# Kernel tuning notes

Hardware: AMD Instinct MI355X
Metric: run time of the kernel (lower is better)

The kernel has to match this reference:

```python
import jax, jax.numpy as jnp
import numpy as np
import math

C = 1.0
IN_FEATURES = 512
SCALE = 1.0 / math.sqrt(IN_FEATURES)  # 1/sqrt(input_size) * lr_mul, lr_mul=1
LR_MUL = 1.0
GAIN = math.sqrt(2.0)
EPS = 1e-5       # clamp epsilon used by hyptorch-style pmath
PROJ_EPS = 1e-3  # boundary epsilon for project()


def _norm(x):
    return jnp.linalg.norm(x, axis=-1, keepdims=True)


def _artanh(x):
    return jnp.arctanh(jnp.clip(x, -1.0 + EPS, 1.0 - EPS))


def _project(x, c):
    sqrt_c = c ** 0.5
    norm = jnp.maximum(_norm(x), EPS)
    maxnorm = (1.0 - PROJ_EPS) / sqrt_c
    return jnp.where(norm > maxnorm, x / norm * maxnorm, x)


def _expmap0(u, c):
    sqrt_c = c ** 0.5
    u_norm = jnp.maximum(_norm(u), EPS)
    return jnp.tanh(sqrt_c * u_norm) * u / (sqrt_c * u_norm)


def _mobius_add(x, y, c):
    x2 = jnp.sum(x * x, axis=-1, keepdims=True)
    y2 = jnp.sum(y * y, axis=-1, keepdims=True)
    xy = jnp.sum(x * y, axis=-1, keepdims=True)
    num = (1.0 + 2.0 * c * xy + c * y2) * x + (1.0 - c * x2) * y
    denom = 1.0 + 2.0 * c * xy + c * c * x2 * y2
    return num / (denom + EPS)


def _mobius_matvec(m, x, c):
    # m: [out, in], x: [N, in]
    sqrt_c = c ** 0.5
    x_norm = jnp.maximum(_norm(x), EPS)
    mx = x @ m.T  # [N, out]
    mx_norm = jnp.maximum(_norm(mx), EPS)
    res = jnp.tanh(mx_norm / x_norm * _artanh(sqrt_c * x_norm)) * mx / (mx_norm * sqrt_c)
    zero_row = jnp.all(mx == 0, axis=-1, keepdims=True)
    return jnp.where(zero_row, jnp.zeros_like(res), res)


def _mobius_scalar_mult(x, r, c):
    sqrt_c = c ** 0.5
    x_norm = jnp.maximum(_norm(x), EPS)
    return jnp.tanh(r * _artanh(sqrt_c * x_norm)) * x / (x_norm * sqrt_c)


def setup_inputs() -> dict:
    key = jax.random.key(0)
    k1, k2, k3 = jax.random.split(key, 3)
    N, D_IN, D_OUT = 131072, 512, 512
    # scale x so points lie well inside the unit Poincare ball (norm ~ 0.45)
    x = jax.random.normal(k1, (N, D_IN), dtype=jnp.float32) * 0.02
    weight = jax.random.normal(k2, (D_OUT, D_IN), dtype=jnp.float32)
    bias = jax.random.normal(k3, (D_OUT,), dtype=jnp.float32) * 0.01
    return {"x": x, "weight": weight, "bias": bias}


def reference(x, weight, bias):
    c = C
    mv = _mobius_matvec(weight * SCALE, x, c)
    b = _expmap0(bias * LR_MUL, c)
    out = _project(_mobius_add(mv, b[None, :], c), c)
    out = jax.nn.leaky_relu(out, 0.2)
    out = _mobius_scalar_mult(out, GAIN, c)
    return out
```

## Files before the change

kernel.cpp:

```cpp
#include <hip/hip_runtime.h>
#include <math.h>

#define EPSV 1e-5f
#define SCALE_W 0.0441941738241592f
#define GAIN_R 1.4142135623730951f

typedef __attribute__((ext_vector_type(8))) short bf16x8;
typedef __attribute__((ext_vector_type(4))) float f32x4;
typedef __attribute__((ext_vector_type(4))) unsigned int u32x4;

static __device__ __forceinline__ unsigned short f2bf(float f) {
  union { float f; unsigned int u; } v; v.f = f;
  unsigned int r = v.u + 0x7FFFu + ((v.u >> 16) & 1u);
  return (unsigned short)(r >> 16);
}

#define GLD_LDS16(gsrc, ldst)                                                                      \
  __builtin_amdgcn_global_load_lds((const __attribute__((address_space(1))) unsigned int*)(gsrc),  \
                                   (__attribute__((address_space(3))) unsigned int*)(ldst), 16, 0, 0)

#define LBAR() do {                                          \
  asm volatile("s_waitcnt lgkmcnt(0)" ::: "memory");         \
  __builtin_amdgcn_sched_barrier(0);                         \
  __builtin_amdgcn_s_barrier();                              \
  __builtin_amdgcn_sched_barrier(0);                         \
} while (0)

#define VMCNT(N) do {                                        \
  asm volatile("s_waitcnt vmcnt(" #N ")" ::: "memory");      \
  __builtin_amdgcn_sched_barrier(0);                         \
} while (0)

__global__ void bias_expmap_k(const float* __restrict__ bias, float* __restrict__ bexp,
                              float* __restrict__ y2out) {
  __shared__ float part[8];
  int t = threadIdx.x;
  float bv = bias[t];
  float s = bv * bv;
  s += __shfl_xor(s, 1);  s += __shfl_xor(s, 2);  s += __shfl_xor(s, 4);
  s += __shfl_xor(s, 8);  s += __shfl_xor(s, 16); s += __shfl_xor(s, 32);
  if ((t & 63) == 0) part[t >> 6] = s;
  __syncthreads();
  float tot = 0.f;
#pragma unroll
  for (int i = 0; i < 8; ++i) tot += part[i];
  float un = fmaxf(sqrtf(tot), EPSV);
  float th = tanhf(un);
  bexp[t] = th * bv / un;
  if (t == 0) *y2out = th * th;
}

__global__ void pack_weight_k(const float* __restrict__ w, unsigned short* __restrict__ wsB) {
  int e = blockIdx.x * 256 + threadIdx.x;
  int o = e >> 9;
  int k = e & 511;
  int ks = k >> 5, kk = k & 31;
  int lgr = kk >> 3, j = kk & 7;
  int colhi = o >> 4, l15 = o & 15;
  int dst = ((ks * 32 + colhi) * 64 + lgr * 16 + l15) * 8 + j;
  wsB[dst] = f2bf(w[e] * SCALE_W);
}

#define RB 80
#define ABUF 5120
#define BOFF 10240
#define BBUF 32768
#define SCR 75776
#define SMEMSZ 80896

__global__ __launch_bounds__(256, 2)
void hyp_main_k(const float* __restrict__ x, const unsigned short* __restrict__ wsB,
                const float* __restrict__ bexp, const float* __restrict__ y2p,
                float* __restrict__ out, int tilesPerBlk) {
  extern __shared__ char smem[];
  const int tid  = threadIdx.x;
  const int lane = tid & 63;
  const int wave = tid >> 6;
  const int l15  = lane & 15;
  const int lgr  = lane >> 4;
  const int srow = tid >> 2;
  const int sq   = tid & 3;

  float* xn2      = (float*)(smem + SCR);
  float* pS2      = (float*)(smem + SCR + 256);
  float* pSB      = (float*)(smem + SCR + 1280);
  float* g12      = (float*)(smem + SCR + 2304);
  float* bexp_lds = (float*)(smem + SCR + 2816);
  float* y2l      = (float*)(smem + SCR + 4864);

  f32x4 acc[4][8];
#pragma unroll
  for (int mf = 0; mf < 4; ++mf)
#pragma unroll
    for (int nf = 0; nf < 8; ++nf) acc[mf][nf] = f32x4{0.f, 0.f, 0.f, 0.f};

  const long base = (long)blockIdx.x * tilesPerBlk;
  const int U = tilesPerBlk * 16;
  float xss = 0.f;
  f32x4 stA, stB;

  {
    float2 bc = *(const float2*)(bexp + tid * 2);
    *(float2*)(bexp_lds + tid * 2) = bc;
    if (tid == 0) *y2l = *y2p;
    const float* p = x + (size_t)(base * 64 + srow) * 512 + sq * 8;
    f32x4 a = *(const f32x4*)p;
    f32x4 b = *(const f32x4*)(p + 4);
    xss += a[0]*a[0] + a[1]*a[1] + a[2]*a[2] + a[3]*a[3];
    xss += b[0]*b[0] + b[1]*b[1] + b[2]*b[2] + b[3]*b[3];
    u32x4 pk;
    pk[0] = (unsigned int)f2bf(a[0]) | ((unsigned int)f2bf(a[1]) << 16);
    pk[1] = (unsigned int)f2bf(a[2]) | ((unsigned int)f2bf(a[3]) << 16);
    pk[2] = (unsigned int)f2bf(b[0]) | ((unsigned int)f2bf(b[1]) << 16);
    pk[3] = (unsigned int)f2bf(b[2]) | ((unsigned int)f2bf(b[3]) << 16);
    *(u32x4*)(smem + srow * RB + sq * 16) = pk;
#pragma unroll
    for (int i = 0; i < 8; ++i)
      GLD_LDS16((const char*)wsB + (wave * 8 + i) * 1024 + lane * 16,
                smem + BOFF + (wave * 8 + i) * 1024);
  }
  LBAR();

#pragma unroll 1
  for (int t = 0; t < U; ++t) {
    const int cur = t & 1, nxt = cur ^ 1;

    {
      const int gu = (t + 1 < U) ? t + 1 : U - 1;
      const float* p = x + (size_t)((base + (gu >> 4)) * 64 + srow) * 512 + (gu & 15) * 32 + sq * 8;
      stA = *(const f32x4*)p;
      stB = *(const f32x4*)(p + 4);
    }
    {
      const char* bs = (const char*)wsB + (size_t)((t + 1) & 15) * 32768;
      char* bd = smem + BOFF + nxt * BBUF;
#pragma unroll
      for (int i = 0; i < 8; ++i)
        GLD_LDS16(bs + (wave * 8 + i) * 1024 + lane * 16, bd + (wave * 8 + i) * 1024);
    }
    if (t > 0 && (t & 15) == 0) { VMCNT(42); } else { VMCNT(10); }

    {
      const char* ab = smem + cur * ABUF + l15 * RB + lgr * 16;
      const char* bb = smem + BOFF + cur * BBUF + (wave * 8) * 1024 + lane * 16;
      bf16x8 xf[4], wf[8];
#pragma unroll
      for (int mf = 0; mf < 4; ++mf) xf[mf] = *(const bf16x8*)(ab + mf * (16 * RB));
#pragma unroll
      for (int nf = 0; nf < 8; ++nf) wf[nf] = *(const bf16x8*)(bb + nf * 1024);
      __builtin_amdgcn_s_setprio(1);
#pragma unroll
      for (int mf = 0; mf < 4; ++mf)
#pragma unroll
        for (int nf = 0; nf < 8; ++nf)
          acc[mf][nf] = __builtin_amdgcn_mfma_f32_16x16x32_bf16(wf[nf], xf[mf], acc[mf][nf], 0, 0, 0);
      __builtin_amdgcn_s_setprio(0);
    }

    if ((t & 15) == 15) {
      const long trow = (base + (t >> 4)) * 64;

      float xs = xss;
      xs += __shfl_xor(xs, 1); xs += __shfl_xor(xs, 2);
      if (sq == 0) xn2[srow] = xs;
      xss = 0.f;

      f32x4 bvv[8];
#pragma unroll
      for (int nf = 0; nf < 8; ++nf)
        bvv[nf] = *(const f32x4*)(bexp_lds + wave * 128 + nf * 16 + lgr * 4);
      const float y2 = *y2l;

      float s2[4], sb[4];
#pragma unroll
      for (int mf = 0; mf < 4; ++mf) {
        s2[mf] = 0.f; sb[mf] = 0.f;
#pragma unroll
        for (int nf = 0; nf < 8; ++nf)
#pragma unroll
          for (int j = 0; j < 4; ++j) {
            float v = acc[mf][nf][j];
            s2[mf] += v * v;
            sb[mf] += v * bvv[nf][j];
          }
        s2[mf] += __shfl_xor(s2[mf], 16); s2[mf] += __shfl_xor(s2[mf], 32);
        sb[mf] += __shfl_xor(sb[mf], 16); sb[mf] += __shfl_xor(sb[mf], 32);
      }
      if (lane < 16) {
#pragma unroll
        for (int mf = 0; mf < 4; ++mf) {
          pS2[(mf * 16 + l15) * 4 + wave] = s2[mf];
          pSB[(mf * 16 + l15) * 4 + wave] = sb[mf];
        }
      }
      LBAR();

      if (tid < 64) {
        int r = tid;
        float S2 = 0.f, SB = 0.f;
#pragma unroll
        for (int i = 0; i < 4; ++i) { S2 += pS2[r * 4 + i]; SB += pSB[r * 4 + i]; }
        float y2s = *y2l;
        float xn  = fmaxf(sqrtf(xn2[r]), EPSV);
        float mxn = fmaxf(sqrtf(S2), EPSV);
        float f = tanhf((mxn / xn) * atanhf(fminf(xn, 1.f - EPSV))) / mxn;
        float xy = f * SB;
        float x2 = f * f * S2;
        float den = 1.f + 2.f * xy + x2 * y2s + EPSV;
        float g1 = (1.f + 2.f * xy + y2s) * f / den;
        float g2 = (1.f - x2) / den;
        float n1sq = g1 * g1 * S2 + 2.f * g1 * g2 * SB + g2 * g2 * y2s;
        float n1 = fmaxf(sqrtf(fmaxf(n1sq, 0.f)), EPSV);
        if (n1 > 0.999f) { float sc = 0.999f / n1; g1 *= sc; g2 *= sc; }
        g12[r * 2] = g1; g12[r * 2 + 1] = g2;
      }
      LBAR();

      float n2p[4];
#pragma unroll
      for (int mf = 0; mf < 4; ++mf) {
        float g1 = g12[(mf * 16 + l15) * 2], g2 = g12[(mf * 16 + l15) * 2 + 1];
        n2p[mf] = 0.f;
#pragma unroll
        for (int nf = 0; nf < 8; ++nf)
#pragma unroll
          for (int j = 0; j < 4; ++j) {
            float v = g1 * acc[mf][nf][j] + g2 * bvv[nf][j];
            v = v > 0.f ? v : 0.2f * v;
            acc[mf][nf][j] = v;
            n2p[mf] += v * v;
          }
        n2p[mf] += __shfl_xor(n2p[mf], 16); n2p[mf] += __shfl_xor(n2p[mf], 32);
      }
      if (lane < 16) {
#pragma unroll
        for (int mf = 0; mf < 4; ++mf) pS2[(mf * 16 + l15) * 4 + wave] = n2p[mf];
      }
      LBAR();

      if (tid < 64) {
        int r = tid;
        float sn = 0.f;
#pragma unroll
        for (int i = 0; i < 4; ++i) sn += pS2[r * 4 + i];
        float n2 = fmaxf(sqrtf(sn), EPSV);
        xn2[r] = tanhf(GAIN_R * atanhf(fminf(n2, 1.f - EPSV))) / n2;
      }
      LBAR();

#pragma unroll
      for (int mf = 0; mf < 4; ++mf) {
        float tm = xn2[mf * 16 + l15];
#pragma unroll
        for (int nf = 0; nf < 8; ++nf) {
          f32x4 o = acc[mf][nf];
          o[0] *= tm; o[1] *= tm; o[2] *= tm; o[3] *= tm;
          *(f32x4*)(out + (size_t)(trow + mf * 16 + l15) * 512 +
                    wave * 128 + nf * 16 + lgr * 4) = o;
          acc[mf][nf] = f32x4{0.f, 0.f, 0.f, 0.f};
        }
      }
    }

    if ((t & 15) == 15) { VMCNT(40); } else { VMCNT(8); }

    {
      f32x4 a = stA, b = stB;
      xss += a[0]*a[0] + a[1]*a[1] + a[2]*a[2] + a[3]*a[3];
      xss += b[0]*b[0] + b[1]*b[1] + b[2]*b[2] + b[3]*b[3];
      u32x4 pk;
      pk[0] = (unsigned int)f2bf(a[0]) | ((unsigned int)f2bf(a[1]) << 16);
      pk[1] = (unsigned int)f2bf(a[2]) | ((unsigned int)f2bf(a[3]) << 16);
      pk[2] = (unsigned int)f2bf(b[0]) | ((unsigned int)f2bf(b[1]) << 16);
      pk[3] = (unsigned int)f2bf(b[2]) | ((unsigned int)f2bf(b[3]) << 16);
      *(u32x4*)(smem + nxt * ABUF + srow * RB + sq * 16) = pk;
    }
    LBAR();
  }
}

extern "C" void kernel_launch(void* const* d_in, const int* in_sizes, int n_in,
                              void* d_out, int out_size, void* d_ws, size_t ws_size,
                              hipStream_t stream) {
  const float* x    = (const float*)d_in[0];
  const float* w    = (const float*)d_in[1];
  const float* bias = (const float*)d_in[2];
  float* out = (float*)d_out;

  unsigned short* wsB = (unsigned short*)d_ws;
  float* bexp = (float*)((char*)d_ws + 524288);
  float* y2p  = (float*)((char*)d_ws + 524288 + 2048);

  bias_expmap_k<<<dim3(1), dim3(512), 0, stream>>>(bias, bexp, y2p);
  pack_weight_k<<<dim3(1024), dim3(256), 0, stream>>>(w, wsB);

  const int nrows  = in_sizes[0] / 512;
  const int ntiles = nrows / 64;
  const int nblk   = 512;
  const int tpb    = ntiles / nblk;
  hyp_main_k<<<dim3(nblk), dim3(256), SMEMSZ, stream>>>(x, wsB, bexp, y2p, out, tpb);
}
```

Baseline: 177.2 us.

## Deepen x prefetch to a 4-stage register ring and use hardware bf16 pack

The main loop now keeps a four-deep register ring of prefetched x fragments instead of a single stage, so global loads of x are issued several k-steps ahead. The loop is split into an outer per-tile loop with a fully unrolled 16-step inner loop, which makes the ring and buffer indices compile-time constants. The barrier moves to the start of each step with a fixed vmcnt wait. The bf16 conversion switches from a software round-to-nearest routine to the v_cvt_pk_bf16_f32 instruction. The deeper ring holds more live registers, which may lower occupancy, and the full unroll enlarges code size.

Result: slower. 441.0 us (+148.9%).

```diff
diff --git a/kernel.cpp b/kernel.cpp
--- a/kernel.cpp
+++ b/kernel.cpp
@@ -13,6 +13,12 @@
   union { float f; unsigned int u; } v; v.f = f;
   unsigned int r = v.u + 0x7FFFu + ((v.u >> 16) & 1u);
   return (unsigned short)(r >> 16);
+}
+
+static __device__ __forceinline__ unsigned int cvtpk(float lo, float hi) {
+  unsigned int r;
+  asm("v_cvt_pk_bf16_f32 %0, %1, %2" : "=v"(r) : "v"(lo), "v"(hi));
+  return r;
 }
 
 #define GLD_LDS16(gsrc, ldst)                                                                      \
@@ -30,6 +36,8 @@
   asm volatile("s_waitcnt vmcnt(" #N ")" ::: "memory");      \
   __builtin_amdgcn_sched_barrier(0);                         \
 } while (0)
+
+#define SBAR() __builtin_amdgcn_sched_barrier(0)
 
 __global__ void bias_expmap_k(const float* __restrict__ bias, float* __restrict__ bexp,
                               float* __restrict__ y2out) {
@@ -96,186 +104,193 @@
 
   const long base = (long)blockIdx.x * tilesPerBlk;
   const int U = tilesPerBlk * 16;
+  const float* xrow = x + (size_t)(base * 64 + srow) * 512 + sq * 8;
   float xss = 0.f;
-  f32x4 stA, stB;
+  f32x4 ring[4][2];
 
   {
     float2 bc = *(const float2*)(bexp + tid * 2);
+    ring[0][0] = *(const f32x4*)(xrow);
+    ring[0][1] = *(const f32x4*)(xrow + 4);
+    ring[1][0] = *(const f32x4*)(xrow + 32);
+    ring[1][1] = *(const f32x4*)(xrow + 36);
+    float y2v = *y2p;
+    VMCNT(0);
     *(float2*)(bexp_lds + tid * 2) = bc;
-    if (tid == 0) *y2l = *y2p;
-    const float* p = x + (size_t)(base * 64 + srow) * 512 + sq * 8;
-    f32x4 a = *(const f32x4*)p;
-    f32x4 b = *(const f32x4*)(p + 4);
+    if (tid == 0) *y2l = y2v;
+    f32x4 a = ring[0][0], b = ring[0][1];
     xss += a[0]*a[0] + a[1]*a[1] + a[2]*a[2] + a[3]*a[3];
     xss += b[0]*b[0] + b[1]*b[1] + b[2]*b[2] + b[3]*b[3];
     u32x4 pk;
-    pk[0] = (unsigned int)f2bf(a[0]) | ((unsigned int)f2bf(a[1]) << 16);
-    pk[1] = (unsigned int)f2bf(a[2]) | ((unsigned int)f2bf(a[3]) << 16);
-    pk[2] = (unsigned int)f2bf(b[0]) | ((unsigned int)f2bf(b[1]) << 16);
-    pk[3] = (unsigned int)f2bf(b[2]) | ((unsigned int)f2bf(b[3]) << 16);
+    pk[0] = cvtpk(a[0], a[1]); pk[1] = cvtpk(a[2], a[3]);
+    pk[2] = cvtpk(b[0], b[1]); pk[3] = cvtpk(b[2], b[3]);
     *(u32x4*)(smem + srow * RB + sq * 16) = pk;
+    SBAR();
 #pragma unroll
     for (int i = 0; i < 8; ++i)
       GLD_LDS16((const char*)wsB + (wave * 8 + i) * 1024 + lane * 16,
                 smem + BOFF + (wave * 8 + i) * 1024);
+    SBAR();
+    ring[2][0] = *(const f32x4*)(xrow + 64);
+    ring[2][1] = *(const f32x4*)(xrow + 68);
+    ring[3][0] = *(const f32x4*)(xrow + 96);
+    ring[3][1] = *(const f32x4*)(xrow + 100);
+    SBAR();
   }
-  LBAR();
 
 #pragma unroll 1
-  for (int t = 0; t < U; ++t) {
-    const int cur = t & 1, nxt = cur ^ 1;
-
-    {
-      const int gu = (t + 1 < U) ? t + 1 : U - 1;
-      const float* p = x + (size_t)((base + (gu >> 4)) * 64 + srow) * 512 + (gu & 15) * 32 + sq * 8;
-      stA = *(const f32x4*)p;
-      stB = *(const f32x4*)(p + 4);
+  for (int tb = 0; tb < tilesPerBlk; ++tb) {
+#pragma unroll
+    for (int u = 0; u < 16; ++u) {
+      const int t = tb * 16 + u;
+      {
+        const char* bs = (const char*)wsB + (size_t)((u + 1) & 15) * 32768;
+        char* bd = smem + BOFF + ((u + 1) & 1) * BBUF;
+#pragma unroll
+        for (int i = 0; i < 8; ++i)
+          GLD_LDS16(bs + (wave * 8 + i) * 1024 + lane * 16, bd + (wave * 8 + i) * 1024);
+      }
+      SBAR();
+      {
+        int gu = t + 4; if (gu >= U) gu = U - 1;
+        const float* p = xrow + (size_t)(gu >> 4) * 32768 + (gu & 15) * 32;
+        ring[(u + 4) & 3][0] = *(const f32x4*)p;
+        ring[(u + 4) & 3][1] = *(const f32x4*)(p + 4);
+      }
+      SBAR();
+      VMCNT(12);
+      LBAR();
+      {
+        const char* ab = smem + (u & 1) * ABUF + l15 * RB + lgr * 16;
+        const char* bb = smem + BOFF + (u & 1) * BBUF + (wave * 8) * 1024 + lane * 16;
+        bf16x8 xf[4], wf[8];
+#pragma unroll
+        for (int mf = 0; mf < 4; ++mf) xf[mf] = *(const bf16x8*)(ab + mf * (16 * RB));
+#pragma unroll
+        for (int nf = 0; nf < 8; ++nf) wf[nf] = *(const bf16x8*)(bb + nf * 1024);
+        __builtin_amdgcn_s_setprio(1);
+#pragma unroll
+        for (int mf = 0; mf < 4; ++mf)
+#pragma unroll
+          for (int nf = 0; nf < 8; ++nf)
+            acc[mf][nf] = __builtin_amdgcn_mfma_f32_16x16x32_bf16(wf[nf], xf[mf], acc[mf][nf], 0, 0, 0);
+        __builtin_amdgcn_s_setprio(0);
+      }
+
+      if (u == 15) {
+        const long trow = (base + tb) * 64;
+
+        float xs = xss;
+        xs += __shfl_xor(xs, 1); xs += __shfl_xor(xs, 2);
+        if (sq == 0) xn2[srow] = xs;
+        xss = 0.f;
+
+        f32x4 bvv[8];
+#pragma unroll
+        for (int nf = 0; nf < 8; ++nf)
+          bvv[nf] = *(const f32x4*)(bexp_lds + wave * 128 + nf * 16 + lgr * 4);
+
+        float s2[4], sb[4];
+#pragma unroll
+        for (int mf = 0; mf < 4; ++mf) {
+          s2[mf] = 0.f; sb[mf] = 0.f;
+#pragma unroll
+          for (int nf = 0; nf < 8; ++nf)
+#pragma unroll
+            for (int j = 0; j < 4; ++j) {
+              float v = acc[mf][nf][j];
+              s2[mf] += v * v;
+              sb[mf] += v * bvv[nf][j];
+            }
+          s2[mf] += __shfl_xor(s2[mf], 16); s2[mf] += __shfl_xor(s2[mf], 32);
+          sb[mf] += __shfl_xor(sb[mf], 16); sb[mf] += __shfl_xor(sb[mf], 32);
+        }
+        if (lane < 16) {
+#pragma unroll
+          for (int mf = 0; mf < 4; ++mf) {
+            pS2[(mf * 16 + l15) * 4 + wave] = s2[mf];
+            pSB[(mf * 16 + l15) * 4 + wave] = sb[mf];
+          }
+        }
+        LBAR();
+
+        if (tid < 64) {
+          int r = tid;
+          float S2 = 0.f, SB = 0.f;
+#pragma unroll
+          for (int i = 0; i < 4; ++i) { S2 += pS2[r * 4 + i]; SB += pSB[r * 4 + i]; }
+          float y2s = *y2l;
+          float xn  = fmaxf(sqrtf(xn2[r]), EPSV);
+          float mxn = fmaxf(sqrtf(S2), EPSV);
+          float f = tanhf((mxn / xn) * atanhf(fminf(xn, 1.f - EPSV))) / mxn;
+          float xy = f * SB;
+          float x2 = f * f * S2;
+          float den = 1.f + 2.f * xy + x2 * y2s + EPSV;
+          float g1 = (1.f + 2.f * xy + y2s) * f / den;
+          float g2 = (1.f - x2) / den;
+          float n1sq = g1 * g1 * S2 + 2.f * g1 * g2 * SB + g2 * g2 * y2s;
+          float n1 = fmaxf(sqrtf(fmaxf(n1sq, 0.f)), EPSV);
+          if (n1 > 0.999f) { float sc = 0.999f / n1; g1 *= sc; g2 *= sc; }
+          g12[r * 2] = g1; g12[r * 2 + 1] = g2;
+        }
+        LBAR();
+
+        float n2p[4];
+#pragma unroll
+        for (int mf = 0; mf < 4; ++mf) {
+          float g1 = g12[(mf * 16 + l15) * 2], g2 = g12[(mf * 16 + l15) * 2 + 1];
+          n2p[mf] = 0.f;
+#pragma unroll
+          for (int nf = 0; nf < 8; ++nf)
+#pragma unroll
+            for (int j = 0; j < 4; ++j) {
+              float v = g1 * acc[mf][nf][j] + g2 * bvv[nf][j];
+              v = v > 0.f ? v : 0.2f * v;
+              acc[mf][nf][j] = v;
+              n2p[mf] += v * v;
+            }
+          n2p[mf] += __shfl_xor(n2p[mf], 16); n2p[mf] += __shfl_xor(n2p[mf], 32);
+        }
+        if (lane < 16) {
+#pragma unroll
+          for (int mf = 0; mf < 4; ++mf) pS2[(mf * 16 + l15) * 4 + wave] = n2p[mf];
+        }
+        LBAR();
+
+        if (tid < 64) {
+          int r = tid;
+          float sn = 0.f;
+#pragma unroll
+          for (int i = 0; i < 4; ++i) sn += pS2[r * 4 + i];
+          float n2 = fmaxf(sqrtf(sn), EPSV);
+          xn2[r] = tanhf(GAIN_R * atanhf(fminf(n2, 1.f - EPSV))) / n2;
+        }
+        LBAR();
+
+#pragma unroll
+        for (int mf = 0; mf < 4; ++mf) {
+          float tm = xn2[mf * 16 + l15];
+#pragma unroll
+          for (int nf = 0; nf < 8; ++nf) {
+            f32x4 o = acc[mf][nf];
+            o[0] *= tm; o[1] *= tm; o[2] *= tm; o[3] *= tm;
+            *(f32x4*)(out + (size_t)(trow + mf * 16 + l15) * 512 +
+                      wave * 128 + nf * 16 + lgr * 4) = o;
+            acc[mf][nf] = f32x4{0.f, 0.f, 0.f, 0.f};
+          }
+        }
+      }
+
+      {
+        f32x4 a = ring[(u + 1) & 3][0], b = ring[(u + 1) & 3][1];
+        xss += a[0]*a[0] + a[1]*a[1] + a[2]*a[2] + a[3]*a[3];
+        xss += b[0]*b[0] + b[1]*b[1] + b[2]*b[2] + b[3]*b[3];
+        u32x4 pk;
+        pk[0] = cvtpk(a[0], a[1]); pk[1] = cvtpk(a[2], a[3]);
+        pk[2] = cvtpk(b[0], b[1]); pk[3] = cvtpk(b[2], b[3]);
+        *(u32x4*)(smem + ((u + 1) & 1) * ABUF + srow * RB + sq * 16) = pk;
+      }
     }
-    {
-      const char* bs = (const char*)wsB + (size_t)((t + 1) & 15) * 32768;
-      char* bd = smem + BOFF + nxt * BBUF;
-#pragma unroll
-      for (int i = 0; i < 8; ++i)
-        GLD_LDS16(bs + (wave * 8 + i) * 1024 + lane * 16, bd + (wave * 8 + i) * 1024);
-    }
-    if (t > 0 && (t & 15) == 0) { VMCNT(42); } else { VMCNT(10); }
-
-    {
-      const char* ab = smem + cur * ABUF + l15 * RB + lgr * 16;
-      const char* bb = smem + BOFF + cur * BBUF + (wave * 8) * 1024 + lane * 16;
-      bf16x8 xf[4], wf[8];
-#pragma unroll
-      for (int mf = 0; mf < 4; ++mf) xf[mf] = *(const bf16x8*)(ab + mf * (16 * RB));
-#pragma unroll
-      for (int nf = 0; nf < 8; ++nf) wf[nf] = *(const bf16x8*)(bb + nf * 1024);
-      __builtin_amdgcn_s_setprio(1);
-#pragma unroll
-      for (int mf = 0; mf < 4; ++mf)
-#pragma unroll
-        for (int nf = 0; nf < 8; ++nf)
-          acc[mf][nf] = __builtin_amdgcn_mfma_f32_16x16x32_bf16(wf[nf], xf[mf], acc[mf][nf], 0, 0, 0);
-      __builtin_amdgcn_s_setprio(0);
-    }
-
-    if ((t & 15) == 15) {
-      const long trow = (base + (t >> 4)) * 64;
-
-      float xs = xss;
-      xs += __shfl_xor(xs, 1); xs += __shfl_xor(xs, 2);
-      if (sq == 0) xn2[srow] = xs;
-      xss = 0.f;
-
-      f32x4 bvv[8];
-#pragma unroll
-      for (int nf = 0; nf < 8; ++nf)
-        bvv[nf] = *(const f32x4*)(bexp_lds + wave * 128 + nf * 16 + lgr * 4);
-      const float y2 = *y2l;
-
-      float s2[4], sb[4];
-#pragma unroll
-      for (int mf = 0; mf < 4; ++mf) {
-        s2[mf] = 0.f; sb[mf] = 0.f;
-#pragma unroll
-        for (int nf = 0; nf < 8; ++nf)
-#pragma unroll
-          for (int j = 0; j < 4; ++j) {
-            float v = acc[mf][nf][j];
-            s2[mf] += v * v;
-            sb[mf] += v * bvv[nf][j];
-          }
-        s2[mf] += __shfl_xor(s2[mf], 16); s2[mf] += __shfl_xor(s2[mf], 32);
-        sb[mf] += __shfl_xor(sb[mf], 16); sb[mf] += __shfl_xor(sb[mf], 32);
-      }
-      if (lane < 16) {
-#pragma unroll
-        for (int mf = 0; mf < 4; ++mf) {
-          pS2[(mf * 16 + l15) * 4 + wave] = s2[mf];
-          pSB[(mf * 16 + l15) * 4 + wave] = sb[mf];
-        }
-      }
-      LBAR();
-
-      if (tid < 64) {
-        int r = tid;
-        float S2 = 0.f, SB = 0.f;
-#pragma unroll
-        for (int i = 0; i < 4; ++i) { S2 += pS2[r * 4 + i]; SB += pSB[r * 4 + i]; }
-        float y2s = *y2l;
-        float xn  = fmaxf(sqrtf(xn2[r]), EPSV);
-        float mxn = fmaxf(sqrtf(S2), EPSV);
-        float f = tanhf((mxn / xn) * atanhf(fminf(xn, 1.f - EPSV))) / mxn;
-        float xy = f * SB;
-        float x2 = f * f * S2;
-        float den = 1.f + 2.f * xy + x2 * y2s + EPSV;
-        float g1 = (1.f + 2.f * xy + y2s) * f / den;
-        float g2 = (1.f - x2) / den;
-        float n1sq = g1 * g1 * S2 + 2.f * g1 * g2 * SB + g2 * g2 * y2s;
-        float n1 = fmaxf(sqrtf(fmaxf(n1sq, 0.f)), EPSV);
-        if (n1 > 0.999f) { float sc = 0.999f / n1; g1 *= sc; g2 *= sc; }
-        g12[r * 2] = g1; g12[r * 2 + 1] = g2;
-      }
-      LBAR();
-
-      float n2p[4];
-#pragma unroll
-      for (int mf = 0; mf < 4; ++mf) {
-        float g1 = g12[(mf * 16 + l15) * 2], g2 = g12[(mf * 16 + l15) * 2 + 1];
-        n2p[mf] = 0.f;
-#pragma unroll
-        for (int nf = 0; nf < 8; ++nf)
-#pragma unroll
-          for (int j = 0; j < 4; ++j) {
-            float v = g1 * acc[mf][nf][j] + g2 * bvv[nf][j];
-            v = v > 0.f ? v : 0.2f * v;
-            acc[mf][nf][j] = v;
-            n2p[mf] += v * v;
-          }
-        n2p[mf] += __shfl_xor(n2p[mf], 16); n2p[mf] += __shfl_xor(n2p[mf], 32);
-      }
-      if (lane < 16) {
-#pragma unroll
-        for (int mf = 0; mf < 4; ++mf) pS2[(mf * 16 + l15) * 4 + wave] = n2p[mf];
-      }
-      LBAR();
-
-      if (tid < 64) {
-        int r = tid;
-        float sn = 0.f;
-#pragma unroll
-        for (int i = 0; i < 4; ++i) sn += pS2[r * 4 + i];
-        float n2 = fmaxf(sqrtf(sn), EPSV);
-        xn2[r] = tanhf(GAIN_R * atanhf(fminf(n2, 1.f - EPSV))) / n2;
-      }
-      LBAR();
-
-#pragma unroll
-      for (int mf = 0; mf < 4; ++mf) {
-        float tm = xn2[mf * 16 + l15];
-#pragma unroll
-        for (int nf = 0; nf < 8; ++nf) {
-          f32x4 o = acc[mf][nf];
-          o[0] *= tm; o[1] *= tm; o[2] *= tm; o[3] *= tm;
-          *(f32x4*)(out + (size_t)(trow + mf * 16 + l15) * 512 +
-                    wave * 128 + nf * 16 + lgr * 4) = o;
-          acc[mf][nf] = f32x4{0.f, 0.f, 0.f, 0.f};
-        }
-      }
-    }
-
-    if ((t & 15) == 15) { VMCNT(40); } else { VMCNT(8); }
-
-    {
-      f32x4 a = stA, b = stB;
-      xss += a[0]*a[0] + a[1]*a[1] + a[2]*a[2] + a[3]*a[3];
-      xss += b[0]*b[0] + b[1]*b[1] + b[2]*b[2] + b[3]*b[3];
-      u32x4 pk;
-      pk[0] = (unsigned int)f2bf(a[0]) | ((unsigned int)f2bf(a[1]) << 16);
-      pk[1] = (unsigned int)f2bf(a[2]) | ((unsigned int)f2bf(a[3]) << 16);
-      pk[2] = (unsigned int)f2bf(b[0]) | ((unsigned int)f2bf(b[1]) << 16);
-      pk[3] = (unsigned int)f2bf(b[2]) | ((unsigned int)f2bf(b[3]) << 16);
-      *(u32x4*)(smem + nxt * ABUF + srow * RB + sq * 16) = pk;
-    }
-    LBAR();
   }
 }
 
```
